# Performance work log

Measured on AMD Instinct MI355X. Metric: run time of the kernel, lower is better.

The kernel has to match this reference:

```python
import jax, jax.numpy as jnp
import numpy as np

B, L, D_MODEL = 4, 2048, 1024
N_HEADS, FEAT, HEAD_DIM = 16, 16, 64
CHUNK = 128
EPS = 1e-12


def taylor_exp(x):
    """2nd-order Taylor feature map of exp(q.k/sqrt(d)).
    x: (b, h, l, f) -> (b, h, l, 1 + f + f*f)"""
    f = x.shape[-1]
    r2 = jnp.sqrt(jnp.asarray(2.0, x.dtype))
    rd = jnp.sqrt(jnp.asarray(float(f), x.dtype))      # sqrt(d)
    rrd = jnp.sqrt(rd)                                  # d**0.25
    x2 = (x[..., :, None] * x[..., None, :]).reshape(*x.shape[:-1], f * f) / r2
    ones = jnp.ones_like(x[..., :1])
    return jnp.concatenate([ones, x / rrd, x2 / rd], axis=-1)


def setup_inputs() -> dict:
    key = jax.random.key(0)
    k1, k2, k3, k4, k5 = jax.random.split(key, 5)
    s = 0.02
    return {
        "hidden_states": jax.random.normal(k1, (B, L, D_MODEL), jnp.float32),
        "Wq": jax.random.normal(k2, (N_HEADS * FEAT, D_MODEL), jnp.float32) * s,
        "Wk": jax.random.normal(k3, (N_HEADS * FEAT, D_MODEL), jnp.float32) * s,
        "Wv": jax.random.normal(k4, (N_HEADS * HEAD_DIM, D_MODEL), jnp.float32) * s,
        "Wo": jax.random.normal(k5, (D_MODEL, N_HEADS * HEAD_DIM), jnp.float32) * s,
    }


def reference(hidden_states, Wq, Wk, Wv, Wo):
    b, l, _ = hidden_states.shape
    # projections (Linear without bias: x @ W.T)
    q = (hidden_states @ Wq.T).reshape(b, l, N_HEADS, FEAT).transpose(0, 2, 1, 3)
    k = (hidden_states @ Wk.T).reshape(b, l, N_HEADS, FEAT).transpose(0, 2, 1, 3)
    v = (hidden_states @ Wv.T).reshape(b, l, N_HEADS, HEAD_DIM).transpose(0, 2, 1, 3)

    qf = taylor_exp(q)  # (b, h, l, De) with De = 1 + f + f^2 = 273
    kf = taylor_exp(k)
    De = qf.shape[-1]

    # chunked causal linear attention: same math as cumulative kv-state
    n = l // CHUNK
    qc = jnp.moveaxis(qf.reshape(b, N_HEADS, n, CHUNK, De), 2, 0)       # (n,b,h,c,De)
    kc = jnp.moveaxis(kf.reshape(b, N_HEADS, n, CHUNK, De), 2, 0)
    vc = jnp.moveaxis(v.reshape(b, N_HEADS, n, CHUNK, HEAD_DIM), 2, 0)
    mask = jnp.tril(jnp.ones((CHUNK, CHUNK), qf.dtype))

    def step(carry, xs):
        S, z = carry                       # S: (b,h,De,e), z: (b,h,De)
        qi, ki, vi = xs
        attn = jnp.einsum('bhid,bhjd->bhij', qi, ki) * mask
        num = jnp.einsum('bhij,bhje->bhie', attn, vi) \
            + jnp.einsum('bhid,bhde->bhie', qi, S)
        den = attn.sum(-1) + jnp.einsum('bhid,bhd->bhi', qi, z)
        yi = num / (den[..., None] + EPS)
        S = S + jnp.einsum('bhjd,bhje->bhde', ki, vi)
        z = z + ki.sum(2)
        return (S, z), yi

    S0 = jnp.zeros((b, N_HEADS, De, HEAD_DIM), qf.dtype)
    z0 = jnp.zeros((b, N_HEADS, De), qf.dtype)
    _, ys = jax.lax.scan(step, (S0, z0), (qc, kc, vc))
    y = jnp.moveaxis(ys, 0, 2).reshape(b, N_HEADS, l, HEAD_DIM)          # (b,h,l,e)
    y = y.transpose(0, 2, 1, 3).reshape(b, l, N_HEADS * HEAD_DIM)        # (b,l,h*e)
    return y @ Wo.T
```

## Files before the change

### kernel.cpp

```cpp
#include <hip/hip_runtime.h>
#include <hip/hip_bf16.h>

#define BB 4
#define LL 2048
#define DM 1024
#define NH 16
#define FEAT 16
#define HD 64
#define CHUNK 128
#define NCHUNK 16
#define NEXT 80
#define SROW 23040
#define EPS 1e-12f
#define INV_R2RD 0.17677669529663688f
#define QKVLD 1536

typedef short bf16x8_t __attribute__((ext_vector_type(8)));
typedef float f32x4_t  __attribute__((ext_vector_type(4)));

__device__ __forceinline__ float b2f(unsigned short u) {
    union { unsigned int i; float f; } x; x.i = ((unsigned int)u) << 16; return x.f;
}
__device__ __forceinline__ unsigned short f2b(float f) {
    __hip_bfloat16 h = __float2bfloat16(f);
    return *reinterpret_cast<unsigned short*>(&h);
}

__global__ __launch_bounds__(256)
void cast_all(const float* __restrict__ hs, const float* __restrict__ wq,
              const float* __restrict__ wk, const float* __restrict__ wv,
              const float* __restrict__ wo, unsigned short* __restrict__ hs_bf,
              unsigned short* __restrict__ wqkv, unsigned short* __restrict__ wo_bf)
{
    const int i = (blockIdx.x * 256 + threadIdx.x) * 4;
    const float* s; unsigned short* d;
    if (i < 8388608)       { s = hs + i;             d = hs_bf + i; }
    else if (i < 8650752)  { s = wq + (i - 8388608); d = wqkv + (i - 8388608); }
    else if (i < 8912896)  { s = wk + (i - 8650752); d = wqkv + 262144 + (i - 8650752); }
    else if (i < 9961472)  { s = wv + (i - 8912896); d = wqkv + 524288 + (i - 8912896); }
    else if (i < 11010048) { s = wo + (i - 9961472); d = wo_bf + (i - 9961472); }
    else return;
    float4 v = *(const float4*)s;
    ushort4 o; o.x = f2b(v.x); o.y = f2b(v.y); o.z = f2b(v.z); o.w = f2b(v.w);
    *(ushort4*)d = o;
}

template <typename OutT>
__global__ __launch_bounds__(256)
void gemm_bf16(const unsigned short* __restrict__ A, const unsigned short* __restrict__ Bw,
               OutT* __restrict__ C, int M, int N, int K, int lda, int ldb, int ldc)
{
    __shared__ unsigned short As[128 * 32];
    __shared__ unsigned short Bs[128 * 32];
    const int tid  = threadIdx.x;
    const int wave = tid >> 6, lane = tid & 63;
    const int m0 = blockIdx.y * 128, n0 = blockIdx.x * 128;
    const int wm = (wave >> 1) * 64, wn = (wave & 1) * 64;
    const int srow = tid >> 2;
    const int skc  = tid & 3;
    const int ml = lane & 15, qq = lane >> 4;

    f32x4_t acc[4][4];
#pragma unroll
    for (int i = 0; i < 4; ++i)
#pragma unroll
        for (int j = 0; j < 4; ++j) acc[i][j] = (f32x4_t){0.f, 0.f, 0.f, 0.f};

    for (int k0 = 0; k0 < K; k0 += 32) {
#pragma unroll
        for (int p = 0; p < 2; ++p) {
            const int row = p * 64 + srow;
            const unsigned short* ga = A  + (size_t)(m0 + row) * lda + k0 + skc * 8;
            const unsigned short* gb = Bw + (size_t)(n0 + row) * ldb + k0 + skc * 8;
            unsigned short* la = As + (size_t)(p * 64 + wave * 16) * 32;
            unsigned short* lb = Bs + (size_t)(p * 64 + wave * 16) * 32;
            __builtin_amdgcn_global_load_lds((const __attribute__((address_space(1))) void*)ga,
                                             (__attribute__((address_space(3))) void*)la, 16, 0, 0);
            __builtin_amdgcn_global_load_lds((const __attribute__((address_space(1))) void*)gb,
                                             (__attribute__((address_space(3))) void*)lb, 16, 0, 0);
        }
        __syncthreads();
        bf16x8_t af[4], bfr[4];
#pragma unroll
        for (int i = 0; i < 4; ++i) {
            af[i]  = *(const bf16x8_t*)(As + (wm + i * 16 + ml) * 32 + qq * 8);
            bfr[i] = *(const bf16x8_t*)(Bs + (wn + i * 16 + ml) * 32 + qq * 8);
        }
#pragma unroll
        for (int i = 0; i < 4; ++i)
#pragma unroll
            for (int j = 0; j < 4; ++j)
                acc[i][j] = __builtin_amdgcn_mfma_f32_16x16x32_bf16(af[i], bfr[j], acc[i][j], 0, 0, 0);
        __syncthreads();
    }
#pragma unroll
    for (int i = 0; i < 4; ++i) {
        const int rbase = m0 + wm + i * 16 + qq * 4;
#pragma unroll
        for (int j = 0; j < 4; ++j) {
            const int col = n0 + wn + j * 16 + ml;
#pragma unroll
            for (int r = 0; r < 4; ++r) {
                const float v = acc[i][j][r];
                if constexpr (sizeof(OutT) == 2) {
                    ((unsigned short*)C)[(size_t)(rbase + r) * ldc + col] = f2b(v);
                } else {
                    ((float*)C)[(size_t)(rbase + r) * ldc + col] = v;
                }
            }
        }
    }
}

__global__ __launch_bounds__(256)
void state_kernel(const unsigned short* __restrict__ qkv, unsigned short* __restrict__ STg)
{
    __shared__ unsigned short KT[16 * 136];
    __shared__ unsigned short VT[80 * 136];

    const int x = blockIdx.x;
    const int c = x & 15, bh = x >> 4;
    const int b = bh >> 4, h = bh & 15;
    const int tid = threadIdx.x;
    const int wave = tid >> 6, lane = tid & 63;
    const int ml = lane & 15, kg8 = (lane >> 4) * 8;
    const size_t rowbase = (size_t)(b * LL + c * CHUNK);
    const size_t Sbase = (size_t)x * SROW;

    {
        const int row = tid >> 1, half = tid & 1;
        uint4 kv = *(const uint4*)(qkv + (rowbase + row) * QKVLD + 256 + h * 16 + half * 8);
        const unsigned short* kp = (const unsigned short*)&kv;
#pragma unroll
        for (int i = 0; i < 8; ++i) KT[(half * 8 + i) * 136 + row] = kp[i];
#pragma unroll
        for (int cc = 0; cc < 4; ++cc) {
            uint4 vv = *(const uint4*)(qkv + (rowbase + row) * QKVLD + 512 + h * 64 + half * 32 + cc * 8);
            const unsigned short* vp = (const unsigned short*)&vv;
#pragma unroll
            for (int i = 0; i < 8; ++i) VT[(half * 32 + cc * 8 + i) * 136 + row] = vp[i];
        }
        if (half == 0) {
            VT[64 * 136 + row] = 0x3F80;
        } else {
#pragma unroll
            for (int e = 65; e < 80; ++e) VT[e * 136 + row] = 0;
        }
    }
    __syncthreads();

    bf16x8_t bfr[5][4];
#pragma unroll
    for (int nt = 0; nt < 5; ++nt)
#pragma unroll
        for (int ks = 0; ks < 4; ++ks)
            bfr[nt][ks] = *(const bf16x8_t*)&VT[(nt * 16 + ml) * 136 + ks * 32 + kg8];

    for (int mt = wave; mt < 18; mt += 4) {
        const int d = mt * 16 + ml;
        bf16x8_t af[4];
#pragma unroll
        for (int ks = 0; ks < 4; ++ks) {
            const int jb = ks * 32 + kg8;
            unsigned short o[8];
            if (d >= 24 && d < 280) {
                const int e = d - 24, a = e >> 4, bq = e & 15;
                bf16x8_t ka = *(const bf16x8_t*)&KT[a  * 136 + jb];
                bf16x8_t kb = *(const bf16x8_t*)&KT[bq * 136 + jb];
#pragma unroll
                for (int j = 0; j < 8; ++j)
                    o[j] = f2b(b2f((unsigned short)ka[j]) * b2f((unsigned short)kb[j]) * INV_R2RD);
            } else if (d == 0) {
#pragma unroll
                for (int j = 0; j < 8; ++j) o[j] = 0x3F80;
            } else if (d <= 16) {
                bf16x8_t kx = *(const bf16x8_t*)&KT[(d - 1) * 136 + jb];
#pragma unroll
                for (int j = 0; j < 8; ++j) o[j] = f2b(b2f((unsigned short)kx[j]) * 0.5f);
            } else {
#pragma unroll
                for (int j = 0; j < 8; ++j) o[j] = 0;
            }
            af[ks] = *(const bf16x8_t*)o;
        }
        f32x4_t acc[5];
#pragma unroll
        for (int nt = 0; nt < 5; ++nt) acc[nt] = (f32x4_t){0.f, 0.f, 0.f, 0.f};
#pragma unroll
        for (int nt = 0; nt < 5; ++nt)
#pragma unroll
            for (int ks = 0; ks < 4; ++ks)
                acc[nt] = __builtin_amdgcn_mfma_f32_16x16x32_bf16(af[ks], bfr[nt][ks], acc[nt], 0, 0, 0);
#pragma unroll
        for (int nt = 0; nt < 5; ++nt) {
            ushort4 pk;
            pk.x = f2b(acc[nt][0]); pk.y = f2b(acc[nt][1]);
            pk.z = f2b(acc[nt][2]); pk.w = f2b(acc[nt][3]);
            *(ushort4*)(STg + Sbase + (size_t)mt * 1280 + (nt * 16 + ml) * 16 + (lane >> 4) * 4) = pk;
        }
    }
}

__global__ __launch_bounds__(256)
void scan_S(unsigned short* __restrict__ STg) {
    const int bh  = blockIdx.y;
    const int idx = blockIdx.x * 256 + threadIdx.x;
    if (idx >= SROW / 8) return;
    const size_t base = (size_t)bh * NCHUNK * SROW + (size_t)idx * 8;
    float acc[8] = {};
    for (int c = 0; c < NCHUNK; ++c) {
        unsigned short* p = STg + base + (size_t)c * SROW;
        uint4 v = *(const uint4*)p;
        const unsigned short* vp = (const unsigned short*)&v;
        uint4 o;
        unsigned short* op = (unsigned short*)&o;
#pragma unroll
        for (int i = 0; i < 8; ++i) { op[i] = f2b(acc[i]); acc[i] += b2f(vp[i]); }
        *(uint4*)p = o;
    }
}

#define OFF_VT 0
#define OFF_QP 0
#define OFF_KP 5120
#define OFF_A  10880
#define OFF_QS 28288

__global__ __launch_bounds__(256)
void out_kernel(const unsigned short* __restrict__ qkv_ro, const unsigned short* __restrict__ STg,
                unsigned short* __restrict__ qkv_w)
{
    __shared__ unsigned short smem[30336];

    const int x = blockIdx.x;
    const int c = x & 15, bh = x >> 4;
    const int b = bh >> 4, h = bh & 15;
    const int tid = threadIdx.x;
    const int w = tid >> 6, lane = tid & 63;
    const int ml = lane & 15, quad = lane >> 4, kg8 = quad * 8;
    const size_t rowbase = (size_t)(b * LL + c * CHUNK);
    const size_t Sbase = (size_t)x * SROW;

    const unsigned short* stp = STg + Sbase + (size_t)(quad >> 1) * 1280 + (quad & 1) * 8;
    bf16x8_t stf[2][5];
#pragma unroll
    for (int nt = 0; nt < 5; ++nt)
        stf[0][nt] = *(const bf16x8_t*)(stp + (nt * 16 + ml) * 16);

    {
        const int row = tid >> 1, half = tid & 1;
        uint4 qv = *(const uint4*)(qkv_ro + (rowbase + row) * QKVLD + h * 16 + half * 8);
        *(uint4*)&smem[OFF_QP + row * 40 + half * 8] = qv;
        *(uint4*)&smem[OFF_QP + row * 40 + 16 + half * 8] = (uint4){0, 0, 0, 0};
        *(uint4*)&smem[OFF_QS + row * 16 + half * 8] = qv;
        uint4 kv = *(const uint4*)(qkv_ro + (rowbase + row) * QKVLD + 256 + h * 16 + half * 8);
        *(uint4*)&smem[OFF_KP + row * 40 + half * 8] = kv;
        *(uint4*)&smem[OFF_KP + row * 40 + 16 + half * 8] = (uint4){0, 0, 0, 0};
    }
    __syncthreads();

    {
        bf16x8_t q0 = *(const bf16x8_t*)&smem[OFF_QP + (w * 32 + ml) * 40 + kg8];
        bf16x8_t q1 = *(const bf16x8_t*)&smem[OFF_QP + (w * 32 + 16 + ml) * 40 + kg8];
#pragma unroll
        for (int nt = 0; nt < 8; ++nt) {
            bf16x8_t kf = *(const bf16x8_t*)&smem[OFF_KP + (nt * 16 + ml) * 40 + kg8];
            f32x4_t a0 = __builtin_amdgcn_mfma_f32_16x16x32_bf16(q0, kf, (f32x4_t){0,0,0,0}, 0, 0, 0);
            f32x4_t a1 = __builtin_amdgcn_mfma_f32_16x16x32_bf16(q1, kf, (f32x4_t){0,0,0,0}, 0, 0, 0);
            const int j = nt * 16 + ml;
#pragma unroll
            for (int r = 0; r < 4; ++r) {
                int i0 = w * 32 + quad * 4 + r;
                float s0 = a0[r] * 0.25f;
                float v0 = (j <= i0) ? (1.f + s0 + 0.5f * s0 * s0) : 0.f;
                smem[OFF_A + i0 * 136 + j] = f2b(v0);
                int i1 = i0 + 16;
                float s1 = a1[r] * 0.25f;
                float v1 = (j <= i1) ? (1.f + s1 + 0.5f * s1 * s1) : 0.f;
                smem[OFF_A + i1 * 136 + j] = f2b(v1);
            }
        }
    }
    const int r0 = w * 32 + ml, r1 = r0 + 16;
    float qA[16], qB[16];
    {
        bf16x8_t t0 = *(const bf16x8_t*)&smem[OFF_QS + r0 * 16];
        bf16x8_t t1 = *(const bf16x8_t*)&smem[OFF_QS + r0 * 16 + 8];
        bf16x8_t t2 = *(const bf16x8_t*)&smem[OFF_QS + r1 * 16];
        bf16x8_t t3 = *(const bf16x8_t*)&smem[OFF_QS + r1 * 16 + 8];
#pragma unroll
        for (int i = 0; i < 8; ++i) {
            qA[i] = b2f((unsigned short)t0[i]); qA[8 + i] = b2f((unsigned short)t1[i]);
            qB[i] = b2f((unsigned short)t2[i]); qB[8 + i] = b2f((unsigned short)t3[i]);
        }
    }
    __syncthreads();

    {
        const int row = tid >> 1, half = tid & 1;
#pragma unroll
        for (int cc = 0; cc < 4; ++cc) {
            uint4 vv = *(const uint4*)(qkv_ro + (rowbase + row) * QKVLD + 512 + h * 64 + half * 32 + cc * 8);
            const unsigned short* vp = (const unsigned short*)&vv;
#pragma unroll
            for (int i = 0; i < 8; ++i) smem[OFF_VT + (half * 32 + cc * 8 + i) * 136 + row] = vp[i];
        }
        if (half == 0) {
            smem[OFF_VT + 64 * 136 + row] = 0x3F80;
        } else {
#pragma unroll
            for (int e = 65; e < 80; ++e) smem[OFF_VT + e * 136 + row] = 0;
        }
    }
    __syncthreads();

    f32x4_t acc[2][5];
#pragma unroll
    for (int mt = 0; mt < 2; ++mt)
#pragma unroll
        for (int nt = 0; nt < 5; ++nt) acc[mt][nt] = (f32x4_t){0.f, 0.f, 0.f, 0.f};

#pragma unroll
    for (int ks = 0; ks < 4; ++ks) {
        bf16x8_t af0 = *(const bf16x8_t*)&smem[OFF_A + (w * 32 + ml) * 136 + ks * 32 + kg8];
        bf16x8_t af1 = *(const bf16x8_t*)&smem[OFF_A + (w * 32 + 16 + ml) * 136 + ks * 32 + kg8];
#pragma unroll
        for (int nt = 0; nt < 5; ++nt) {
            bf16x8_t bv = *(const bf16x8_t*)&smem[OFF_VT + (nt * 16 + ml) * 136 + ks * 32 + kg8];
            acc[0][nt] = __builtin_amdgcn_mfma_f32_16x16x32_bf16(af0, bv, acc[0][nt], 0, 0, 0);
            acc[1][nt] = __builtin_amdgcn_mfma_f32_16x16x32_bf16(af1, bv, acc[1][nt], 0, 0, 0);
        }
    }

#pragma unroll
    for (int kq = 0; kq < 9; ++kq) {
        if (kq < 8) {
#pragma unroll
            for (int nt = 0; nt < 5; ++nt)
                stf[(kq + 1) & 1][nt] =
                    *(const bf16x8_t*)(stp + (size_t)(kq + 1) * 2560 + (nt * 16 + ml) * 16);
        }
        bf16x8_t qf[2];
#pragma unroll
        for (int mt = 0; mt < 2; ++mt) {
            const float* q = (mt == 0) ? qA : qB;
            const int qsrow = (mt == 0) ? r0 : r1;
            const int d0 = kq * 32 + kg8;
            unsigned short o[8];
            if (d0 >= 24 && d0 < 280) {
                const int e0 = d0 - 24;
                const float qa = b2f(smem[OFF_QS + qsrow * 16 + (e0 >> 4)]) * INV_R2RD;
                if ((e0 & 15) == 0) {
#pragma unroll
                    for (int j = 0; j < 8; ++j) o[j] = f2b(qa * q[j]);
                } else {
#pragma unroll
                    for (int j = 0; j < 8; ++j) o[j] = f2b(qa * q[8 + j]);
                }
            } else if (d0 == 0) {
                o[0] = 0x3F80;
#pragma unroll
                for (int j = 1; j < 8; ++j) o[j] = f2b(q[j - 1] * 0.5f);
            } else if (d0 == 8) {
#pragma unroll
                for (int j = 0; j < 8; ++j) o[j] = f2b(q[7 + j] * 0.5f);
            } else if (d0 == 16) {
                o[0] = f2b(q[15] * 0.5f);
#pragma unroll
                for (int j = 1; j < 8; ++j) o[j] = 0;
            } else {
#pragma unroll
                for (int j = 0; j < 8; ++j) o[j] = 0;
            }
            qf[mt] = *(const bf16x8_t*)o;
        }
#pragma unroll
        for (int nt = 0; nt < 5; ++nt) {
            acc[0][nt] = __builtin_amdgcn_mfma_f32_16x16x32_bf16(qf[0], stf[kq & 1][nt], acc[0][nt], 0, 0, 0);
            acc[1][nt] = __builtin_amdgcn_mfma_f32_16x16x32_bf16(qf[1], stf[kq & 1][nt], acc[1][nt], 0, 0, 0);
        }
    }

#pragma unroll
    for (int mt = 0; mt < 2; ++mt) {
        float den[4];
#pragma unroll
        for (int r = 0; r < 4; ++r) den[r] = __shfl(acc[mt][4][r], lane & 48);
#pragma unroll
        for (int r = 0; r < 4; ++r) {
            const size_t grow = rowbase + w * 32 + mt * 16 + quad * 4 + r;
            const float rc = 1.f / (den[r] + EPS);
#pragma unroll
            for (int nt = 0; nt < 4; ++nt)
                qkv_w[grow * QKVLD + 512 + h * 64 + nt * 16 + ml] = f2b(acc[mt][nt][r] * rc);
        }
    }
}

extern "C" void kernel_launch(void* const* d_in, const int* in_sizes, int n_in,
                              void* d_out, int out_size, void* d_ws, size_t ws_size,
                              hipStream_t stream)
{
    (void)in_sizes; (void)n_in; (void)out_size; (void)ws_size;
    const float* hs = (const float*)d_in[0];
    const float* Wq = (const float*)d_in[1];
    const float* Wk = (const float*)d_in[2];
    const float* Wv = (const float*)d_in[3];
    const float* Wo = (const float*)d_in[4];
    float* out = (float*)d_out;

    const int M = BB * LL;
    char* ws = (char*)d_ws;
    unsigned short* STg   = (unsigned short*)ws;
    unsigned short* hs_bf = (unsigned short*)ws;
    size_t off = 47185920;
    unsigned short* qkv   = (unsigned short*)(ws + off); off += 25165824;
    unsigned short* Wqkv  = (unsigned short*)(ws + off); off += 3145728;
    unsigned short* Wo_bf = (unsigned short*)(ws + off); off += 2097152;

    cast_all<<<10752, 256, 0, stream>>>(hs, Wq, Wk, Wv, Wo, hs_bf, Wqkv, Wo_bf);
    gemm_bf16<unsigned short><<<dim3(12, 64), 256, 0, stream>>>(hs_bf, Wqkv, qkv,
                                                                M, 1536, DM, DM, DM, QKVLD);
    state_kernel<<<1024, 256, 0, stream>>>(qkv, STg);
    scan_S<<<dim3(12, 64), 256, 0, stream>>>(STg);
    out_kernel<<<1024, 256, 0, stream>>>(qkv, STg, qkv);
    gemm_bf16<float><<<dim3(8, 64), 256, 0, stream>>>(qkv + 512, Wo_bf, out,
                                                      M, DM, DM, QKVLD, DM, DM);
}
```

Baseline: 217.5 us.

## Fuse hidden-state bf16 cast into QKV GEMM and swizzle LDS tiles

```diff
diff --git a/kernel.cpp b/kernel.cpp
--- a/kernel.cpp
+++ b/kernel.cpp
@@ -27,18 +27,16 @@
 }
 
 __global__ __launch_bounds__(256)
-void cast_all(const float* __restrict__ hs, const float* __restrict__ wq,
-              const float* __restrict__ wk, const float* __restrict__ wv,
-              const float* __restrict__ wo, unsigned short* __restrict__ hs_bf,
-              unsigned short* __restrict__ wqkv, unsigned short* __restrict__ wo_bf)
+void cast_w(const float* __restrict__ wq, const float* __restrict__ wk,
+            const float* __restrict__ wv, const float* __restrict__ wo,
+            unsigned short* __restrict__ wqkv, unsigned short* __restrict__ wo_bf)
 {
     const int i = (blockIdx.x * 256 + threadIdx.x) * 4;
     const float* s; unsigned short* d;
-    if (i < 8388608)       { s = hs + i;             d = hs_bf + i; }
-    else if (i < 8650752)  { s = wq + (i - 8388608); d = wqkv + (i - 8388608); }
-    else if (i < 8912896)  { s = wk + (i - 8650752); d = wqkv + 262144 + (i - 8650752); }
-    else if (i < 9961472)  { s = wv + (i - 8912896); d = wqkv + 524288 + (i - 8912896); }
-    else if (i < 11010048) { s = wo + (i - 9961472); d = wo_bf + (i - 9961472); }
+    if (i < 262144)       { s = wq + i;             d = wqkv + i; }
+    else if (i < 524288)  { s = wk + (i - 262144);  d = wqkv + i; }
+    else if (i < 1572864) { s = wv + (i - 524288);  d = wqkv + i; }
+    else if (i < 2621440) { s = wo + (i - 1572864); d = wo_bf + (i - 1572864); }
     else return;
     float4 v = *(const float4*)s;
     ushort4 o; o.x = f2b(v.x); o.y = f2b(v.y); o.z = f2b(v.z); o.w = f2b(v.w);
@@ -58,6 +56,7 @@
     const int wm = (wave >> 1) * 64, wn = (wave & 1) * 64;
     const int srow = tid >> 2;
     const int skc  = tid & 3;
+    const int gkc  = skc ^ ((srow >> 1) & 3);
     const int ml = lane & 15, qq = lane >> 4;
 
     f32x4_t acc[4][4];
@@ -70,8 +69,8 @@
 #pragma unroll
         for (int p = 0; p < 2; ++p) {
             const int row = p * 64 + srow;
-            const unsigned short* ga = A  + (size_t)(m0 + row) * lda + k0 + skc * 8;
-            const unsigned short* gb = Bw + (size_t)(n0 + row) * ldb + k0 + skc * 8;
+            const unsigned short* ga = A  + (size_t)(m0 + row) * lda + k0 + gkc * 8;
+            const unsigned short* gb = Bw + (size_t)(n0 + row) * ldb + k0 + gkc * 8;
             unsigned short* la = As + (size_t)(p * 64 + wave * 16) * 32;
             unsigned short* lb = Bs + (size_t)(p * 64 + wave * 16) * 32;
             __builtin_amdgcn_global_load_lds((const __attribute__((address_space(1))) void*)ga,
@@ -83,8 +82,9 @@
         bf16x8_t af[4], bfr[4];
 #pragma unroll
         for (int i = 0; i < 4; ++i) {
-            af[i]  = *(const bf16x8_t*)(As + (wm + i * 16 + ml) * 32 + qq * 8);
-            bfr[i] = *(const bf16x8_t*)(Bs + (wn + i * 16 + ml) * 32 + qq * 8);
+            const int ra = wm + i * 16 + ml, rb = wn + i * 16 + ml;
+            af[i]  = *(const bf16x8_t*)(As + ra * 32 + (qq ^ ((ra >> 1) & 3)) * 8);
+            bfr[i] = *(const bf16x8_t*)(Bs + rb * 32 + (qq ^ ((rb >> 1) & 3)) * 8);
         }
 #pragma unroll
         for (int i = 0; i < 4; ++i)
@@ -108,6 +108,71 @@
                     ((float*)C)[(size_t)(rbase + r) * ldc + col] = v;
                 }
             }
+        }
+    }
+}
+
+__global__ __launch_bounds__(256)
+void gemm_qkv(const float* __restrict__ A, const unsigned short* __restrict__ Bw,
+              unsigned short* __restrict__ C, int M, int N, int K, int lda, int ldb, int ldc)
+{
+    __shared__ unsigned short As[128 * 32];
+    __shared__ unsigned short Bs[128 * 32];
+    const int tid  = threadIdx.x;
+    const int wave = tid >> 6, lane = tid & 63;
+    const int m0 = blockIdx.y * 128, n0 = blockIdx.x * 128;
+    const int wm = (wave >> 1) * 64, wn = (wave & 1) * 64;
+    const int srow = tid >> 2;
+    const int skc  = tid & 3;
+    const int gkc  = skc ^ ((srow >> 1) & 3);
+    const int ml = lane & 15, qq = lane >> 4;
+
+    f32x4_t acc[4][4];
+#pragma unroll
+    for (int i = 0; i < 4; ++i)
+#pragma unroll
+        for (int j = 0; j < 4; ++j) acc[i][j] = (f32x4_t){0.f, 0.f, 0.f, 0.f};
+
+    for (int k0 = 0; k0 < K; k0 += 32) {
+#pragma unroll
+        for (int p = 0; p < 2; ++p) {
+            const int row = p * 64 + srow;
+            const float* gaf = A + (size_t)(m0 + row) * lda + k0 + gkc * 8;
+            float4 a0 = *(const float4*)gaf;
+            float4 a1 = *(const float4*)(gaf + 4);
+            unsigned short pk[8];
+            pk[0] = f2b(a0.x); pk[1] = f2b(a0.y); pk[2] = f2b(a0.z); pk[3] = f2b(a0.w);
+            pk[4] = f2b(a1.x); pk[5] = f2b(a1.y); pk[6] = f2b(a1.z); pk[7] = f2b(a1.w);
+            *(bf16x8_t*)(As + (size_t)(p * 64 + srow) * 32 + skc * 8) = *(const bf16x8_t*)pk;
+            const unsigned short* gb = Bw + (size_t)(n0 + row) * ldb + k0 + gkc * 8;
+            unsigned short* lb = Bs + (size_t)(p * 64 + wave * 16) * 32;
+            __builtin_amdgcn_global_load_lds((const __attribute__((address_space(1))) void*)gb,
+                                             (__attribute__((address_space(3))) void*)lb, 16, 0, 0);
+        }
+        __syncthreads();
+        bf16x8_t af[4], bfr[4];
+#pragma unroll
+        for (int i = 0; i < 4; ++i) {
+            const int ra = wm + i * 16 + ml, rb = wn + i * 16 + ml;
+            af[i]  = *(const bf16x8_t*)(As + ra * 32 + (qq ^ ((ra >> 1) & 3)) * 8);
+            bfr[i] = *(const bf16x8_t*)(Bs + rb * 32 + (qq ^ ((rb >> 1) & 3)) * 8);
+        }
+#pragma unroll
+        for (int i = 0; i < 4; ++i)
+#pragma unroll
+            for (int j = 0; j < 4; ++j)
+                acc[i][j] = __builtin_amdgcn_mfma_f32_16x16x32_bf16(af[i], bfr[j], acc[i][j], 0, 0, 0);
+        __syncthreads();
+    }
+#pragma unroll
+    for (int i = 0; i < 4; ++i) {
+        const int rbase = m0 + wm + i * 16 + qq * 4;
+#pragma unroll
+        for (int j = 0; j < 4; ++j) {
+            const int col = n0 + wn + j * 16 + ml;
+#pragma unroll
+            for (int r = 0; r < 4; ++r)
+                C[(size_t)(rbase + r) * ldc + col] = f2b(acc[i][j][r]);
         }
     }
 }
@@ -412,15 +477,13 @@
     const int M = BB * LL;
     char* ws = (char*)d_ws;
     unsigned short* STg   = (unsigned short*)ws;
-    unsigned short* hs_bf = (unsigned short*)ws;
     size_t off = 47185920;
     unsigned short* qkv   = (unsigned short*)(ws + off); off += 25165824;
     unsigned short* Wqkv  = (unsigned short*)(ws + off); off += 3145728;
     unsigned short* Wo_bf = (unsigned short*)(ws + off); off += 2097152;
 
-    cast_all<<<10752, 256, 0, stream>>>(hs, Wq, Wk, Wv, Wo, hs_bf, Wqkv, Wo_bf);
-    gemm_bf16<unsigned short><<<dim3(12, 64), 256, 0, stream>>>(hs_bf, Wqkv, qkv,
-                                                                M, 1536, DM, DM, DM, QKVLD);
+    cast_w<<<2560, 256, 0, stream>>>(Wq, Wk, Wv, Wo, Wqkv, Wo_bf);
+    gemm_qkv<<<dim3(12, 64), 256, 0, stream>>>(hs, Wqkv, qkv, M, 1536, DM, DM, DM, QKVLD);
     state_kernel<<<1024, 256, 0, stream>>>(qkv, STg);
     scan_S<<<dim3(12, 64), 256, 0, stream>>>(STg);
     out_kernel<<<1024, 256, 0, stream>>>(qkv, STg, qkv);
```

New measurement: 222.7 us. +2.4%, slower.
